# Performance work log

Measured on AMD Instinct MI355X. Metric: run time of the kernel, lower is better.

The kernel has to match this reference:

```python
import jax, jax.numpy as jnp
import numpy as np

N = 20000        # num nodes
E = 600000       # num edges (avg degree 30)
H_DIM = 128      # num_hidden
NUM_IN = 256     # edge feature dim = 2*num_hidden
HEADS = 4
D = H_DIM // HEADS  # per-head dim = 32


def _lin_init(key, out_dim, in_dim):
    return (jax.random.normal(key, (out_dim, in_dim), dtype=jnp.float32)
            * (1.0 / np.sqrt(in_dim)))


def setup_inputs() -> dict:
    key = jax.random.key(0)
    ks = jax.random.split(key, 12)
    h_V = jax.random.normal(ks[0], (N, H_DIM), dtype=jnp.float32)
    h_E = jax.random.normal(ks[1], (E, NUM_IN), dtype=jnp.float32)
    center_id = jax.random.randint(ks[2], (E,), 0, N)
    batch_id = jnp.zeros((N,), dtype=jnp.int32)  # unused by the math
    # W_V: num_in->h, h->h, h->h (GELU between first two pairs)
    Wv1 = _lin_init(ks[3], H_DIM, NUM_IN); bv1 = jnp.zeros((H_DIM,), jnp.float32)
    Wv2 = _lin_init(ks[4], H_DIM, H_DIM);  bv2 = jnp.zeros((H_DIM,), jnp.float32)
    Wv3 = _lin_init(ks[5], H_DIM, H_DIM);  bv3 = jnp.zeros((H_DIM,), jnp.float32)
    # Bias: 3h->h, h->h, h->heads
    Wb1 = _lin_init(ks[6], H_DIM, 3 * H_DIM); bb1 = jnp.zeros((H_DIM,), jnp.float32)
    Wb2 = _lin_init(ks[7], H_DIM, H_DIM);     bb2 = jnp.zeros((H_DIM,), jnp.float32)
    Wb3 = _lin_init(ks[8], HEADS, H_DIM);     bb3 = jnp.zeros((HEADS,), jnp.float32)
    # W_O: h->h, no bias
    Wo = _lin_init(ks[9], H_DIM, H_DIM)
    return {"h_V": h_V, "h_E": h_E,
            "Wv1": Wv1, "bv1": bv1, "Wv2": Wv2, "bv2": bv2, "Wv3": Wv3, "bv3": bv3,
            "Wb1": Wb1, "bb1": bb1, "Wb2": Wb2, "bb2": bb2, "Wb3": Wb3, "bb3": bb3,
            "Wo": Wo, "center_id": center_id, "batch_id": batch_id}


def _gelu(x):
    return jax.nn.gelu(x, approximate=False)  # torch nn.GELU default (erf)


def reference(h_V, h_E, Wv1, bv1, Wv2, bv2, Wv3, bv3,
              Wb1, bb1, Wb2, bb2, Wb3, bb3, Wo, center_id, batch_id):
    n = h_V.shape[0]
    # Bias MLP on gathered node feats + edge feats -> per-edge per-head logit
    x = jnp.concatenate([h_V[center_id], h_E], axis=-1)          # (E, 3h)
    w = _gelu(x @ Wb1.T + bb1)
    w = _gelu(w @ Wb2.T + bb2)
    w = (w @ Wb3.T + bb3) * (1.0 / np.sqrt(D))                   # (E, heads)
    # Value MLP on edge feats
    V = _gelu(h_E @ Wv1.T + bv1)
    V = _gelu(V @ Wv2.T + bv2)
    V = (V @ Wv3.T + bv3).reshape(-1, HEADS, D)                  # (E, heads, d)
    # scatter_softmax over edges sharing a center node
    m = jax.ops.segment_max(w, center_id, num_segments=n)        # (N, heads)
    ew = jnp.exp(w - m[center_id])                               # (E, heads)
    denom = jax.ops.segment_sum(ew, center_id, num_segments=n)   # (N, heads)
    attend = ew / denom[center_id]                               # (E, heads)
    # scatter_sum aggregate of attention-weighted values
    agg = jax.ops.segment_sum(attend[:, :, None] * V, center_id,
                              num_segments=n).reshape(n, H_DIM)  # (N, h)
    return agg @ Wo.T                                            # W_O, no bias
```

## Files before the change

### kernel.cpp

```cpp
#include <hip/hip_runtime.h>
#include <hip/hip_bf16.h>
#include <math.h>

#define TE 32
#define XS 392
#define HS 264
#define NTILES 18750

typedef __attribute__((ext_vector_type(8))) short bf16x8;
typedef __attribute__((ext_vector_type(4))) float f32x4;

__device__ __forceinline__ unsigned short f2b(float f) {
    unsigned int x = __float_as_uint(f);
    unsigned int r = x + 0x7fffu + ((x >> 16) & 1u);
    return (unsigned short)(r >> 16);
}
__device__ __forceinline__ float b2f(unsigned short u) {
    return __uint_as_float(((unsigned int)u) << 16);
}
__device__ __forceinline__ float gelu_exact(float v) {
    return 0.5f * v * (1.0f + erff(v * 0.70710678118654752f));
}

__global__ void __launch_bounds__(256)
k_pre(const float* __restrict__ Wb1, const float* __restrict__ Wb2,
      const float* __restrict__ Wv1, const float* __restrict__ Wv2,
      const float* __restrict__ Wv3, const float* __restrict__ Wo,
      unsigned short* __restrict__ wbf, float* __restrict__ woT) {
    int t = blockIdx.x * 256 + threadIdx.x;
    if (t < 49152)       wbf[t] = f2b(Wb1[t]);
    else if (t < 65536)  wbf[t] = f2b(Wb2[t - 49152]);
    else if (t < 98304)  wbf[t] = f2b(Wv1[t - 65536]);
    else if (t < 114688) wbf[t] = f2b(Wv2[t - 98304]);
    else if (t < 131072) wbf[t] = f2b(Wv3[t - 114688]);
    else if (t < 147456) {
        int i = t - 131072; int j = i >> 7, k = i & 127;
        woT[k * 128 + j] = Wo[j * 128 + k];
    }
}

__global__ void __launch_bounds__(256)
k_hist(const int* __restrict__ center, int* __restrict__ counts) {
    int t = blockIdx.x * 256 + threadIdx.x;
    if (t < 600000) atomicAdd(&counts[center[t]], 1);
}

__global__ void __launch_bounds__(256)
k_scan(const int* __restrict__ counts, int* __restrict__ offsets,
       int* __restrict__ cursor, int n) {
    __shared__ int buf[256];
    __shared__ int carry;
    int t = threadIdx.x;
    if (t == 0) carry = 0;
    __syncthreads();
    for (int base = 0; base < n; base += 256) {
        int v = (base + t < n) ? counts[base + t] : 0;
        buf[t] = v; __syncthreads();
        for (int off = 1; off < 256; off <<= 1) {
            int x = (t >= off) ? buf[t - off] : 0;
            __syncthreads();
            buf[t] += x;
            __syncthreads();
        }
        int excl = carry + buf[t] - v;
        if (base + t < n) { offsets[base + t] = excl; cursor[base + t] = excl; }
        int tot = buf[255];
        __syncthreads();
        if (t == 0) carry += tot;
        __syncthreads();
    }
}

__global__ void __launch_bounds__(256)
k_place(const int* __restrict__ center, int* __restrict__ cursor, int* __restrict__ eidx) {
    int t = blockIdx.x * 256 + threadIdx.x;
    if (t < 600000) {
        int p = atomicAdd(&cursor[center[t]], 1);
        eidx[p] = t;
    }
}

__device__ __forceinline__ void stage_tile(int t, int eg0,
        const float* __restrict__ hE, const float* __restrict__ hV,
        const int* __restrict__ center, unsigned short* __restrict__ xs) {
    #pragma unroll
    for (int i = 0; i < 4; ++i) {
        int vid = t + i * 512;
        int e = vid >> 6, kq = vid & 63;
        float4 g = *(const float4*)(hE + (size_t)(eg0 + e) * 256 + kq * 4);
        ushort4 p; p.x = f2b(g.x); p.y = f2b(g.y); p.z = f2b(g.z); p.w = f2b(g.w);
        *(ushort4*)&xs[e * XS + 128 + kq * 4] = p;
    }
    #pragma unroll
    for (int i = 0; i < 2; ++i) {
        int vid = t + i * 512;
        int e = vid >> 5, kq = vid & 31;
        int c = center[eg0 + e];
        float4 g = *(const float4*)(hV + (size_t)c * 128 + kq * 4);
        ushort4 p; p.x = f2b(g.x); p.y = f2b(g.y); p.z = f2b(g.z); p.w = f2b(g.w);
        *(ushort4*)&xs[e * XS + kq * 4] = p;
    }
}

__global__ void __launch_bounds__(512, 2)
k_edge(const float* __restrict__ hV, const float* __restrict__ hE,
       const int* __restrict__ center,
       const float* __restrict__ bv1, const float* __restrict__ bv2, const float* __restrict__ bv3,
       const float* __restrict__ bb1, const float* __restrict__ bb2,
       const float* __restrict__ Wb3, const float* __restrict__ bb3,
       const unsigned short* __restrict__ wbf,
       unsigned short* __restrict__ Vbf, float* __restrict__ ew, float* __restrict__ denom)
{
    __shared__ unsigned short smem[29440];
    __shared__ float wb3s[512];
    const int t = threadIdx.x;
    const int wave = t >> 6, lane = t & 63;
    const int c16 = lane & 15, q = lane >> 4;
    wb3s[t] = Wb3[t];

    unsigned short* xs = smem;
    unsigned short* h1 = smem + 12544;
    unsigned short* h2 = smem + 20992;

    const unsigned short* Wb1bf = wbf;
    const unsigned short* Wb2bf = wbf + 49152;
    const unsigned short* Wv1bf = wbf + 65536;
    const unsigned short* Wv2bf = wbf + 98304;
    const unsigned short* Wv3bf = wbf + 114688;

    if (wave < 4) {
        const int fb = wave * 32;
        bf16x8 wb1[2][12], wb2[2][4];
        float bias1[2], bias2[2];
        #pragma unroll
        for (int nt = 0; nt < 2; ++nt) {
            const int fr = fb + nt * 16 + c16;
            #pragma unroll
            for (int ks = 0; ks < 12; ++ks)
                wb1[nt][ks] = *(const bf16x8*)(Wb1bf + (size_t)fr * 384 + ks * 32 + q * 8);
            #pragma unroll
            for (int ks = 0; ks < 4; ++ks)
                wb2[nt][ks] = *(const bf16x8*)(Wb2bf + (size_t)fr * 128 + ks * 32 + q * 8);
            bias1[nt] = bb1[fr]; bias2[nt] = bb2[fr];
        }
        for (int tile = blockIdx.x; tile < NTILES; tile += gridDim.x) {
            const int eg0 = tile * TE;
            stage_tile(t, eg0, hE, hV, center, xs);
            __syncthreads();
            #pragma unroll
            for (int m = 0; m < 2; ++m) {
                bf16x8 af[12];
                #pragma unroll
                for (int ks = 0; ks < 12; ++ks)
                    af[ks] = *(const bf16x8*)&xs[(m * 16 + c16) * XS + ks * 32 + q * 8];
                f32x4 a0 = {0.f,0.f,0.f,0.f}, a1 = {0.f,0.f,0.f,0.f};
                #pragma unroll
                for (int ks = 0; ks < 12; ++ks) {
                    a0 = __builtin_amdgcn_mfma_f32_16x16x32_bf16(af[ks], wb1[0][ks], a0, 0, 0, 0);
                    a1 = __builtin_amdgcn_mfma_f32_16x16x32_bf16(af[ks], wb1[1][ks], a1, 0, 0, 0);
                }
                #pragma unroll
                for (int r = 0; r < 4; ++r) {
                    int row = (m * 16 + q * 4 + r) * HS;
                    h1[row + fb + c16]      = f2b(gelu_exact(a0[r] + bias1[0]));
                    h1[row + fb + 16 + c16] = f2b(gelu_exact(a1[r] + bias1[1]));
                }
            }
            __syncthreads();
            #pragma unroll
            for (int m = 0; m < 2; ++m) {
                bf16x8 ah[4];
                #pragma unroll
                for (int ks = 0; ks < 4; ++ks)
                    ah[ks] = *(const bf16x8*)&h1[(m * 16 + c16) * HS + ks * 32 + q * 8];
                f32x4 a0 = {0.f,0.f,0.f,0.f}, a1 = {0.f,0.f,0.f,0.f};
                #pragma unroll
                for (int ks = 0; ks < 4; ++ks) {
                    a0 = __builtin_amdgcn_mfma_f32_16x16x32_bf16(ah[ks], wb2[0][ks], a0, 0, 0, 0);
                    a1 = __builtin_amdgcn_mfma_f32_16x16x32_bf16(ah[ks], wb2[1][ks], a1, 0, 0, 0);
                }
                #pragma unroll
                for (int r = 0; r < 4; ++r) {
                    int row = (m * 16 + q * 4 + r) * HS;
                    h2[row + fb + c16]      = f2b(gelu_exact(a0[r] + bias2[0]));
                    h2[row + fb + 16 + c16] = f2b(gelu_exact(a1[r] + bias2[1]));
                }
            }
            __syncthreads();
            if (t < 128) {
                const int e = t & 31, head = t >> 5;
                float acc = 0.f;
                #pragma unroll
                for (int kc = 0; kc < 16; ++kc) {
                    bf16x8 h = *(const bf16x8*)&h2[e * HS + kc * 8];
                    #pragma unroll
                    for (int j = 0; j < 8; ++j)
                        acc += b2f((unsigned short)h[j]) * wb3s[head * 128 + kc * 8 + j];
                }
                float w = (acc + bb3[head]) * 0.17677669529663689f;
                float xv = expf(w);
                ew[(size_t)(eg0 + e) * 4 + head] = xv;
                atomicAdd(&denom[(size_t)center[eg0 + e] * 4 + head], xv);
            }
        }
    } else {
        const int fv = (wave - 4) * 32;
        bf16x8 wv1[2][8], wv2[2][4], wv3[2][4];
        float bias1[2], bias2[2], bias3[2];
        #pragma unroll
        for (int nt = 0; nt < 2; ++nt) {
            const int fr = fv + nt * 16 + c16;
            #pragma unroll
            for (int ks = 0; ks < 8; ++ks)
                wv1[nt][ks] = *(const bf16x8*)(Wv1bf + (size_t)fr * 256 + ks * 32 + q * 8);
            #pragma unroll
            for (int ks = 0; ks < 4; ++ks) {
                wv2[nt][ks] = *(const bf16x8*)(Wv2bf + (size_t)fr * 128 + ks * 32 + q * 8);
                wv3[nt][ks] = *(const bf16x8*)(Wv3bf + (size_t)fr * 128 + ks * 32 + q * 8);
            }
            bias1[nt] = bv1[fr]; bias2[nt] = bv2[fr]; bias3[nt] = bv3[fr];
        }
        for (int tile = blockIdx.x; tile < NTILES; tile += gridDim.x) {
            const int eg0 = tile * TE;
            stage_tile(t, eg0, hE, hV, center, xs);
            __syncthreads();
            #pragma unroll
            for (int m = 0; m < 2; ++m) {
                bf16x8 af[8];
                #pragma unroll
                for (int ks = 0; ks < 8; ++ks)
                    af[ks] = *(const bf16x8*)&xs[(m * 16 + c16) * XS + 128 + ks * 32 + q * 8];
                f32x4 a0 = {0.f,0.f,0.f,0.f}, a1 = {0.f,0.f,0.f,0.f};
                #pragma unroll
                for (int ks = 0; ks < 8; ++ks) {
                    a0 = __builtin_amdgcn_mfma_f32_16x16x32_bf16(af[ks], wv1[0][ks], a0, 0, 0, 0);
                    a1 = __builtin_amdgcn_mfma_f32_16x16x32_bf16(af[ks], wv1[1][ks], a1, 0, 0, 0);
                }
                #pragma unroll
                for (int r = 0; r < 4; ++r) {
                    int row = (m * 16 + q * 4 + r) * HS;
                    h1[row + 128 + fv + c16]      = f2b(gelu_exact(a0[r] + bias1[0]));
                    h1[row + 128 + fv + 16 + c16] = f2b(gelu_exact(a1[r] + bias1[1]));
                }
            }
            __syncthreads();
            #pragma unroll
            for (int m = 0; m < 2; ++m) {
                bf16x8 ah[4];
                #pragma unroll
                for (int ks = 0; ks < 4; ++ks)
                    ah[ks] = *(const bf16x8*)&h1[(m * 16 + c16) * HS + 128 + ks * 32 + q * 8];
                f32x4 a0 = {0.f,0.f,0.f,0.f}, a1 = {0.f,0.f,0.f,0.f};
                #pragma unroll
                for (int ks = 0; ks < 4; ++ks) {
                    a0 = __builtin_amdgcn_mfma_f32_16x16x32_bf16(ah[ks], wv2[0][ks], a0, 0, 0, 0);
                    a1 = __builtin_amdgcn_mfma_f32_16x16x32_bf16(ah[ks], wv2[1][ks], a1, 0, 0, 0);
                }
                #pragma unroll
                for (int r = 0; r < 4; ++r) {
                    int row = (m * 16 + q * 4 + r) * HS;
                    h2[row + 128 + fv + c16]      = f2b(gelu_exact(a0[r] + bias2[0]));
                    h2[row + 128 + fv + 16 + c16] = f2b(gelu_exact(a1[r] + bias2[1]));
                }
            }
            __syncthreads();
            #pragma unroll
            for (int m = 0; m < 2; ++m) {
                bf16x8 av[4];
                #pragma unroll
                for (int ks = 0; ks < 4; ++ks)
                    av[ks] = *(const bf16x8*)&h2[(m * 16 + c16) * HS + 128 + ks * 32 + q * 8];
                f32x4 a0 = {0.f,0.f,0.f,0.f}, a1 = {0.f,0.f,0.f,0.f};
                #pragma unroll
                for (int ks = 0; ks < 4; ++ks) {
                    a0 = __builtin_amdgcn_mfma_f32_16x16x32_bf16(av[ks], wv3[0][ks], a0, 0, 0, 0);
                    a1 = __builtin_amdgcn_mfma_f32_16x16x32_bf16(av[ks], wv3[1][ks], a1, 0, 0, 0);
                }
                #pragma unroll
                for (int r = 0; r < 4; ++r) {
                    size_t row = (size_t)(eg0 + m * 16 + q * 4 + r) * 128;
                    Vbf[row + fv + c16]      = f2b(a0[r] + bias3[0]);
                    Vbf[row + fv + 16 + c16] = f2b(a1[r] + bias3[1]);
                }
            }
        }
    }
}

__global__ void __launch_bounds__(256)
k_gather_out(const unsigned short* __restrict__ Vbf, const float* __restrict__ ew,
             const float* __restrict__ denom, const int* __restrict__ offsets,
             const int* __restrict__ counts, const int* __restrict__ eidx,
             const float* __restrict__ woT, float* __restrict__ out)
{
    __shared__ float aggs[4][128];
    const int t = threadIdx.x;
    const int node = blockIdx.x * 4 + (t >> 6);
    const int lane = t & 63;
    const int j = lane * 2, head = j >> 5;
    {
        int off = offsets[node], deg = counts[node];
        float den = denom[(size_t)node * 4 + head];
        float dinv = (den != 0.f) ? (1.f / den) : 0.f;
        float a0 = 0.f, a1 = 0.f;
        for (int i = 0; i < deg; ++i) {
            int e = eidx[off + i];
            float at = ew[(size_t)e * 4 + head] * dinv;
            ushort2 v = *(const ushort2*)(Vbf + (size_t)e * 128 + j);
            a0 += at * b2f(v.x);
            a1 += at * b2f(v.y);
        }
        aggs[t >> 6][j]     = a0;
        aggs[t >> 6][j + 1] = a1;
    }
    __syncthreads();
    {
        const int c = t & 127, nh = t >> 7;
        float o0 = 0.f, o1 = 0.f;
        for (int k = 0; k < 128; ++k) {
            float w = woT[k * 128 + c];
            o0 += w * aggs[nh][k];
            o1 += w * aggs[nh + 2][k];
        }
        out[(size_t)(blockIdx.x * 4 + nh) * 128 + c]     = o0;
        out[(size_t)(blockIdx.x * 4 + nh + 2) * 128 + c] = o1;
    }
}

extern "C" void kernel_launch(void* const* d_in, const int* in_sizes, int n_in,
                              void* d_out, int out_size, void* d_ws, size_t ws_size,
                              hipStream_t stream) {
    const float* hV  = (const float*)d_in[0];
    const float* hE  = (const float*)d_in[1];
    const float* Wv1 = (const float*)d_in[2];
    const float* bv1 = (const float*)d_in[3];
    const float* Wv2 = (const float*)d_in[4];
    const float* bv2 = (const float*)d_in[5];
    const float* Wv3 = (const float*)d_in[6];
    const float* bv3 = (const float*)d_in[7];
    const float* Wb1 = (const float*)d_in[8];
    const float* bb1 = (const float*)d_in[9];
    const float* Wb2 = (const float*)d_in[10];
    const float* bb2 = (const float*)d_in[11];
    const float* Wb3 = (const float*)d_in[12];
    const float* bb3 = (const float*)d_in[13];
    const float* Wo  = (const float*)d_in[14];
    const int* center = (const int*)d_in[15];
    float* out = (float*)d_out;

    char* ws = (char*)d_ws;
    unsigned short* wbf = (unsigned short*)(ws + 0);
    float* woT     = (float*)(ws + 262144);
    float* denom   = (float*)(ws + 327680);
    int*   counts  = (int*)  (ws + 647680);
    int*   offsets = (int*)  (ws + 727680);
    int*   cursor  = (int*)  (ws + 807680);
    int*   eidx    = (int*)  (ws + 887680);
    float* ew      = (float*)(ws + 3287680);
    unsigned short* Vbf = (unsigned short*)(ws + 12887680);

    hipMemsetAsync(ws + 327680, 0, 400000, stream);
    k_pre  <<<576, 256, 0, stream>>>(Wb1, Wb2, Wv1, Wv2, Wv3, Wo, wbf, woT);
    k_hist <<<2344, 256, 0, stream>>>(center, counts);
    k_scan <<<1, 256, 0, stream>>>(counts, offsets, cursor, 20000);
    k_place<<<2344, 256, 0, stream>>>(center, cursor, eidx);
    k_edge <<<512, 512, 0, stream>>>(hV, hE, center, bv1, bv2, bv3,
                                     bb1, bb2, Wb3, bb3, wbf, Vbf, ew, denom);
    k_gather_out<<<5000, 256, 0, stream>>>(Vbf, ew, denom, offsets, counts, eidx, woT, out);
}
```

Before: 1.473 ms.

## Precompute per-node bias projection, process edges in sorted order, prefetch tiles, fast GELU

The node half of the first bias layer is precomputed once per node (k_pnode) and gathered per edge, which shrinks the edge GEMM K from 384 to 256 and the staging buffer. Edges are processed in center-sorted order so the aggregation kernel reads V and ew contiguously without the eidx indirection. Next-tile global loads are prefetched into registers, and the bias output layer now uses MFMA. Exact erf GELU is replaced by an Abramowitz-Stegun polynomial, the scan is parallelised, and the occupancy hint and grid size go up. The GELU approximation and bf16 node projection add numerical error, and the gathered edge loads are less coalesced.

```diff
diff --git a/kernel.cpp b/kernel.cpp
--- a/kernel.cpp
+++ b/kernel.cpp
@@ -3,7 +3,7 @@
 #include <math.h>
 
 #define TE 32
-#define XS 392
+#define XS 264
 #define HS 264
 #define NTILES 18750
 
@@ -18,25 +18,58 @@
 __device__ __forceinline__ float b2f(unsigned short u) {
     return __uint_as_float(((unsigned int)u) << 16);
 }
-__device__ __forceinline__ float gelu_exact(float v) {
-    return 0.5f * v * (1.0f + erff(v * 0.70710678118654752f));
+__device__ __forceinline__ float gelu_fast(float v) {
+    float x = fabsf(v) * 0.70710678118654752f;
+    float t = __builtin_amdgcn_rcpf(1.0f + 0.3275911f * x);
+    float p = ((((1.061405429f * t - 1.453152027f) * t + 1.421413741f) * t
+                - 0.284496736f) * t + 0.254829592f) * t;
+    float e = __expf(-x * x);
+    float erfp = 1.0f - p * e;
+    return 0.5f * v * (1.0f + copysignf(erfp, v));
 }
 
 __global__ void __launch_bounds__(256)
 k_pre(const float* __restrict__ Wb1, const float* __restrict__ Wb2,
       const float* __restrict__ Wv1, const float* __restrict__ Wv2,
-      const float* __restrict__ Wv3, const float* __restrict__ Wo,
+      const float* __restrict__ Wv3, const float* __restrict__ Wb3,
+      const float* __restrict__ Wo,
       unsigned short* __restrict__ wbf, float* __restrict__ woT) {
     int t = blockIdx.x * 256 + threadIdx.x;
-    if (t < 49152)       wbf[t] = f2b(Wb1[t]);
-    else if (t < 65536)  wbf[t] = f2b(Wb2[t - 49152]);
-    else if (t < 98304)  wbf[t] = f2b(Wv1[t - 65536]);
-    else if (t < 114688) wbf[t] = f2b(Wv2[t - 98304]);
-    else if (t < 131072) wbf[t] = f2b(Wv3[t - 114688]);
-    else if (t < 147456) {
-        int i = t - 131072; int j = i >> 7, k = i & 127;
+    if (t < 32768) { int f = t >> 8, k = t & 255; wbf[t] = f2b(Wb1[f * 384 + 128 + k]); }
+    else if (t < 49152)  wbf[t] = f2b(Wb2[t - 32768]);
+    else if (t < 81920)  wbf[t] = f2b(Wv1[t - 49152]);
+    else if (t < 98304)  wbf[t] = f2b(Wv2[t - 81920]);
+    else if (t < 114688) wbf[t] = f2b(Wv3[t - 98304]);
+    else if (t < 116736) {
+        int i = t - 114688; int r = i >> 7, k = i & 127;
+        wbf[t] = (r < 4) ? f2b(Wb3[r * 128 + k]) : (unsigned short)0;
+    } else if (t < 133120) {
+        int i = t - 116736; int j = i >> 7, k = i & 127;
         woT[k * 128 + j] = Wo[j * 128 + k];
     }
+}
+
+__global__ void __launch_bounds__(256)
+k_pnode(const float* __restrict__ hV, const float* __restrict__ Wb1,
+        const float* __restrict__ bb1, unsigned short* __restrict__ Pbf) {
+    const int t = threadIdx.x;
+    const int lane = t & 63;
+    const int node = blockIdx.x * 4 + (t >> 6);
+    const int f0 = lane * 2;
+    const float* hv = hV + (size_t)node * 128;
+    const float* w0 = Wb1 + (size_t)f0 * 384;
+    const float* w1 = w0 + 384;
+    float a0 = 0.f, a1 = 0.f;
+    #pragma unroll 4
+    for (int kk = 0; kk < 32; ++kk) {
+        float4 h  = *(const float4*)(hv + kk * 4);
+        float4 x0 = *(const float4*)(w0 + kk * 4);
+        float4 x1 = *(const float4*)(w1 + kk * 4);
+        a0 += h.x * x0.x + h.y * x0.y + h.z * x0.z + h.w * x0.w;
+        a1 += h.x * x1.x + h.y * x1.y + h.z * x1.z + h.w * x1.w;
+    }
+    ushort2 p; p.x = f2b(a0 + bb1[f0]); p.y = f2b(a1 + bb1[f0 + 1]);
+    *(ushort2*)&Pbf[(size_t)node * 128 + f0] = p;
 }
 
 __global__ void __launch_bounds__(256)
@@ -45,29 +78,34 @@
     if (t < 600000) atomicAdd(&counts[center[t]], 1);
 }
 
-__global__ void __launch_bounds__(256)
-k_scan(const int* __restrict__ counts, int* __restrict__ offsets,
-       int* __restrict__ cursor, int n) {
-    __shared__ int buf[256];
-    __shared__ int carry;
-    int t = threadIdx.x;
-    if (t == 0) carry = 0;
+__global__ void __launch_bounds__(1024)
+k_scan(const int* __restrict__ counts, int* __restrict__ cursor, int n) {
+    __shared__ int wtot[16];
+    const int t = threadIdx.x, lane = t & 63, w = t >> 6;
+    const int CH = 20;
+    const int base = t * CH;
+    int loc[CH]; int s = 0;
+    #pragma unroll
+    for (int i = 0; i < CH; ++i) {
+        int idx = base + i;
+        int v = (idx < n) ? counts[idx] : 0;
+        loc[i] = s; s += v;
+    }
+    int inc = s;
+    for (int o = 1; o < 64; o <<= 1) { int u = __shfl_up(inc, o); if (lane >= o) inc += u; }
+    if (lane == 63) wtot[w] = inc;
     __syncthreads();
-    for (int base = 0; base < n; base += 256) {
-        int v = (base + t < n) ? counts[base + t] : 0;
-        buf[t] = v; __syncthreads();
-        for (int off = 1; off < 256; off <<= 1) {
-            int x = (t >= off) ? buf[t - off] : 0;
-            __syncthreads();
-            buf[t] += x;
-            __syncthreads();
-        }
-        int excl = carry + buf[t] - v;
-        if (base + t < n) { offsets[base + t] = excl; cursor[base + t] = excl; }
-        int tot = buf[255];
-        __syncthreads();
-        if (t == 0) carry += tot;
-        __syncthreads();
+    if (w == 0 && lane < 16) {
+        int v = wtot[lane]; int p = v;
+        for (int o = 1; o < 16; o <<= 1) { int u = __shfl_up(p, o); if (lane >= o) p += u; }
+        wtot[lane] = p - v;
+    }
+    __syncthreads();
+    const int excl = wtot[w] + inc - s;
+    #pragma unroll
+    for (int i = 0; i < CH; ++i) {
+        int idx = base + i;
+        if (idx < n) cursor[idx] = excl + loc[i];
     }
 }
 
@@ -80,90 +118,105 @@
     }
 }
 
-__device__ __forceinline__ void stage_tile(int t, int eg0,
-        const float* __restrict__ hE, const float* __restrict__ hV,
-        const int* __restrict__ center, unsigned short* __restrict__ xs) {
-    #pragma unroll
-    for (int i = 0; i < 4; ++i) {
-        int vid = t + i * 512;
-        int e = vid >> 6, kq = vid & 63;
-        float4 g = *(const float4*)(hE + (size_t)(eg0 + e) * 256 + kq * 4);
-        ushort4 p; p.x = f2b(g.x); p.y = f2b(g.y); p.z = f2b(g.z); p.w = f2b(g.w);
-        *(ushort4*)&xs[e * XS + 128 + kq * 4] = p;
-    }
-    #pragma unroll
-    for (int i = 0; i < 2; ++i) {
-        int vid = t + i * 512;
-        int e = vid >> 5, kq = vid & 31;
-        int c = center[eg0 + e];
-        float4 g = *(const float4*)(hV + (size_t)c * 128 + kq * 4);
-        ushort4 p; p.x = f2b(g.x); p.y = f2b(g.y); p.z = f2b(g.z); p.w = f2b(g.w);
-        *(ushort4*)&xs[e * XS + kq * 4] = p;
-    }
-}
-
-__global__ void __launch_bounds__(512, 2)
-k_edge(const float* __restrict__ hV, const float* __restrict__ hE,
-       const int* __restrict__ center,
-       const float* __restrict__ bv1, const float* __restrict__ bv2, const float* __restrict__ bv3,
-       const float* __restrict__ bb1, const float* __restrict__ bb2,
-       const float* __restrict__ Wb3, const float* __restrict__ bb3,
-       const unsigned short* __restrict__ wbf,
+#define PREFETCH(eg) { \
+    int e0_ = eidx[(eg) + wave];      int e1_ = eidx[(eg) + wave + 8]; \
+    int e2_ = eidx[(eg) + wave + 16]; int e3_ = eidx[(eg) + wave + 24]; \
+    if (t < 32) pc = center[eidx[(eg) + t]]; \
+    pre[0] = *(const float4*)(hE + (size_t)e0_ * 256 + kq4); \
+    pre[1] = *(const float4*)(hE + (size_t)e1_ * 256 + kq4); \
+    pre[2] = *(const float4*)(hE + (size_t)e2_ * 256 + kq4); \
+    pre[3] = *(const float4*)(hE + (size_t)e3_ * 256 + kq4); }
+
+#define STAGE() { \
+    _Pragma("unroll") \
+    for (int i_ = 0; i_ < 4; ++i_) { \
+        ushort4 p_; p_.x = f2b(pre[i_].x); p_.y = f2b(pre[i_].y); \
+        p_.z = f2b(pre[i_].z); p_.w = f2b(pre[i_].w); \
+        *(ushort4*)&xs[(wave + i_ * 8) * XS + kq4] = p_; } \
+    if (t < 32) cs[t] = pc; }
+
+__global__ void __launch_bounds__(512, 6)
+k_edge(const float* __restrict__ hE, const int* __restrict__ center,
+       const int* __restrict__ eidx, const unsigned short* __restrict__ Pbf,
+       const float* __restrict__ bv1, const float* __restrict__ bv2,
+       const float* __restrict__ bv3, const float* __restrict__ bb2,
+       const float* __restrict__ bb3, const unsigned short* __restrict__ wbf,
        unsigned short* __restrict__ Vbf, float* __restrict__ ew, float* __restrict__ denom)
 {
-    __shared__ unsigned short smem[29440];
-    __shared__ float wb3s[512];
+    __shared__ unsigned short smem[25344];
+    __shared__ int cs[32];
     const int t = threadIdx.x;
     const int wave = t >> 6, lane = t & 63;
     const int c16 = lane & 15, q = lane >> 4;
-    wb3s[t] = Wb3[t];
+    const int kq4 = (t & 63) * 4;
 
     unsigned short* xs = smem;
-    unsigned short* h1 = smem + 12544;
-    unsigned short* h2 = smem + 20992;
+    unsigned short* h1 = smem + 8448;
+    unsigned short* h2 = smem + 16896;
 
     const unsigned short* Wb1bf = wbf;
-    const unsigned short* Wb2bf = wbf + 49152;
-    const unsigned short* Wv1bf = wbf + 65536;
-    const unsigned short* Wv2bf = wbf + 98304;
-    const unsigned short* Wv3bf = wbf + 114688;
+    const unsigned short* Wb2bf = wbf + 32768;
+    const unsigned short* Wv1bf = wbf + 49152;
+    const unsigned short* Wv2bf = wbf + 81920;
+    const unsigned short* Wv3bf = wbf + 98304;
+    const unsigned short* Wb3bf = wbf + 114688;
+
+    float4 pre[4]; int pc = 0;
+    PREFETCH(blockIdx.x * TE);
 
     if (wave < 4) {
         const int fb = wave * 32;
-        bf16x8 wb1[2][12], wb2[2][4];
-        float bias1[2], bias2[2];
+        bf16x8 wb1r[2][8], wb2r[2][4], wb3f[4];
+        float bias2[2]; float bb3c = 0.f;
         #pragma unroll
         for (int nt = 0; nt < 2; ++nt) {
             const int fr = fb + nt * 16 + c16;
             #pragma unroll
-            for (int ks = 0; ks < 12; ++ks)
-                wb1[nt][ks] = *(const bf16x8*)(Wb1bf + (size_t)fr * 384 + ks * 32 + q * 8);
+            for (int ks = 0; ks < 8; ++ks)
+                wb1r[nt][ks] = *(const bf16x8*)(Wb1bf + (size_t)fr * 256 + ks * 32 + q * 8);
             #pragma unroll
             for (int ks = 0; ks < 4; ++ks)
-                wb2[nt][ks] = *(const bf16x8*)(Wb2bf + (size_t)fr * 128 + ks * 32 + q * 8);
-            bias1[nt] = bb1[fr]; bias2[nt] = bb2[fr];
+                wb2r[nt][ks] = *(const bf16x8*)(Wb2bf + (size_t)fr * 128 + ks * 32 + q * 8);
+            bias2[nt] = bb2[fr];
+        }
+        if (wave == 0) {
+            #pragma unroll
+            for (int ks = 0; ks < 4; ++ks)
+                wb3f[ks] = *(const bf16x8*)(Wb3bf + (size_t)c16 * 128 + ks * 32 + q * 8);
+            bb3c = bb3[c16 & 3];
         }
         for (int tile = blockIdx.x; tile < NTILES; tile += gridDim.x) {
             const int eg0 = tile * TE;
-            stage_tile(t, eg0, hE, hV, center, xs);
-            __syncthreads();
+            STAGE();
+            int nxt = tile + gridDim.x;
+            if (nxt < NTILES) PREFETCH(nxt * TE);
+            __syncthreads();
+            float pva[2][2][4];
+            #pragma unroll
+            for (int m = 0; m < 2; ++m)
+                #pragma unroll
+                for (int r = 0; r < 4; ++r) {
+                    int c = cs[m * 16 + q * 4 + r];
+                    pva[m][0][r] = b2f(Pbf[(size_t)c * 128 + fb + c16]);
+                    pva[m][1][r] = b2f(Pbf[(size_t)c * 128 + fb + 16 + c16]);
+                }
             #pragma unroll
             for (int m = 0; m < 2; ++m) {
-                bf16x8 af[12];
-                #pragma unroll
-                for (int ks = 0; ks < 12; ++ks)
+                bf16x8 af[8];
+                #pragma unroll
+                for (int ks = 0; ks < 8; ++ks)
                     af[ks] = *(const bf16x8*)&xs[(m * 16 + c16) * XS + ks * 32 + q * 8];
                 f32x4 a0 = {0.f,0.f,0.f,0.f}, a1 = {0.f,0.f,0.f,0.f};
                 #pragma unroll
-                for (int ks = 0; ks < 12; ++ks) {
-                    a0 = __builtin_amdgcn_mfma_f32_16x16x32_bf16(af[ks], wb1[0][ks], a0, 0, 0, 0);
-                    a1 = __builtin_amdgcn_mfma_f32_16x16x32_bf16(af[ks], wb1[1][ks], a1, 0, 0, 0);
+                for (int ks = 0; ks < 8; ++ks) {
+                    a0 = __builtin_amdgcn_mfma_f32_16x16x32_bf16(af[ks], wb1r[0][ks], a0, 0, 0, 0);
+                    a1 = __builtin_amdgcn_mfma_f32_16x16x32_bf16(af[ks], wb1r[1][ks], a1, 0, 0, 0);
                 }
                 #pragma unroll
                 for (int r = 0; r < 4; ++r) {
                     int row = (m * 16 + q * 4 + r) * HS;
-                    h1[row + fb + c16]      = f2b(gelu_exact(a0[r] + bias1[0]));
-                    h1[row + fb + 16 + c16] = f2b(gelu_exact(a1[r] + bias1[1]));
+                    h1[row + fb + c16]      = f2b(gelu_fast(a0[r] + pva[m][0][r]));
+                    h1[row + fb + 16 + c16] = f2b(gelu_fast(a1[r] + pva[m][1][r]));
                 }
             }
             __syncthreads();
@@ -176,71 +229,81 @@
                 f32x4 a0 = {0.f,0.f,0.f,0.f}, a1 = {0.f,0.f,0.f,0.f};
                 #pragma unroll
                 for (int ks = 0; ks < 4; ++ks) {
-                    a0 = __builtin_amdgcn_mfma_f32_16x16x32_bf16(ah[ks], wb2[0][ks], a0, 0, 0, 0);
-                    a1 = __builtin_amdgcn_mfma_f32_16x16x32_bf16(ah[ks], wb2[1][ks], a1, 0, 0, 0);
+                    a0 = __builtin_amdgcn_mfma_f32_16x16x32_bf16(ah[ks], wb2r[0][ks], a0, 0, 0, 0);
+                    a1 = __builtin_amdgcn_mfma_f32_16x16x32_bf16(ah[ks], wb2r[1][ks], a1, 0, 0, 0);
                 }
                 #pragma unroll
                 for (int r = 0; r < 4; ++r) {
                     int row = (m * 16 + q * 4 + r) * HS;
-                    h2[row + fb + c16]      = f2b(gelu_exact(a0[r] + bias2[0]));
-                    h2[row + fb + 16 + c16] = f2b(gelu_exact(a1[r] + bias2[1]));
-                }
-            }
-            __syncthreads();
-            if (t < 128) {
-                const int e = t & 31, head = t >> 5;
-                float acc = 0.f;
-                #pragma unroll
-                for (int kc = 0; kc < 16; ++kc) {
-                    bf16x8 h = *(const bf16x8*)&h2[e * HS + kc * 8];
+                    h2[row + fb + c16]      = f2b(gelu_fast(a0[r] + bias2[0]));
+                    h2[row + fb + 16 + c16] = f2b(gelu_fast(a1[r] + bias2[1]));
+                }
+            }
+            __syncthreads();
+            if (wave == 0) {
+                #pragma unroll
+                for (int m = 0; m < 2; ++m) {
+                    bf16x8 ah[4];
                     #pragma unroll
-                    for (int j = 0; j < 8; ++j)
-                        acc += b2f((unsigned short)h[j]) * wb3s[head * 128 + kc * 8 + j];
-                }
-                float w = (acc + bb3[head]) * 0.17677669529663689f;
-                float xv = expf(w);
-                ew[(size_t)(eg0 + e) * 4 + head] = xv;
-                atomicAdd(&denom[(size_t)center[eg0 + e] * 4 + head], xv);
+                    for (int ks = 0; ks < 4; ++ks)
+                        ah[ks] = *(const bf16x8*)&h2[(m * 16 + c16) * HS + ks * 32 + q * 8];
+                    f32x4 a = {0.f,0.f,0.f,0.f};
+                    #pragma unroll
+                    for (int ks = 0; ks < 4; ++ks)
+                        a = __builtin_amdgcn_mfma_f32_16x16x32_bf16(ah[ks], wb3f[ks], a, 0, 0, 0);
+                    if (c16 < 4) {
+                        #pragma unroll
+                        for (int r = 0; r < 4; ++r) {
+                            int row = m * 16 + q * 4 + r;
+                            float wv = (a[r] + bb3c) * 0.17677669529663689f;
+                            float evx = __expf(wv);
+                            ew[(size_t)(eg0 + row) * 4 + c16] = evx;
+                            atomicAdd(&denom[(size_t)cs[row] * 4 + c16], evx);
+                        }
+                    }
+                }
             }
         }
     } else {
         const int fv = (wave - 4) * 32;
-        bf16x8 wv1[2][8], wv2[2][4], wv3[2][4];
-        float bias1[2], bias2[2], bias3[2];
+        bf16x8 wv1r[2][8], wv2r[2][4], wv3r[2][4];
+        float b1[2], b2[2], b3[2];
         #pragma unroll
         for (int nt = 0; nt < 2; ++nt) {
             const int fr = fv + nt * 16 + c16;
             #pragma unroll
             for (int ks = 0; ks < 8; ++ks)
-                wv1[nt][ks] = *(const bf16x8*)(Wv1bf + (size_t)fr * 256 + ks * 32 + q * 8);
+                wv1r[nt][ks] = *(const bf16x8*)(Wv1bf + (size_t)fr * 256 + ks * 32 + q * 8);
             #pragma unroll
             for (int ks = 0; ks < 4; ++ks) {
-                wv2[nt][ks] = *(const bf16x8*)(Wv2bf + (size_t)fr * 128 + ks * 32 + q * 8);
-                wv3[nt][ks] = *(const bf16x8*)(Wv3bf + (size_t)fr * 128 + ks * 32 + q * 8);
-            }
-            bias1[nt] = bv1[fr]; bias2[nt] = bv2[fr]; bias3[nt] = bv3[fr];
+                wv2r[nt][ks] = *(const bf16x8*)(Wv2bf + (size_t)fr * 128 + ks * 32 + q * 8);
+                wv3r[nt][ks] = *(const bf16x8*)(Wv3bf + (size_t)fr * 128 + ks * 32 + q * 8);
+            }
+            b1[nt] = bv1[fr]; b2[nt] = bv2[fr]; b3[nt] = bv3[fr];
         }
         for (int tile = blockIdx.x; tile < NTILES; tile += gridDim.x) {
             const int eg0 = tile * TE;
-            stage_tile(t, eg0, hE, hV, center, xs);
+            STAGE();
+            int nxt = tile + gridDim.x;
+            if (nxt < NTILES) PREFETCH(nxt * TE);
             __syncthreads();
             #pragma unroll
             for (int m = 0; m < 2; ++m) {
                 bf16x8 af[8];
                 #pragma unroll
                 for (int ks = 0; ks < 8; ++ks)
-                    af[ks] = *(const bf16x8*)&xs[(m * 16 + c16) * XS + 128 + ks * 32 + q * 8];
+                    af[ks] = *(const bf16x8*)&xs[(m * 16 + c16) * XS + ks * 32 + q * 8];
                 f32x4 a0 = {0.f,0.f,0.f,0.f}, a1 = {0.f,0.f,0.f,0.f};
                 #pragma unroll
                 for (int ks = 0; ks < 8; ++ks) {
-                    a0 = __builtin_amdgcn_mfma_f32_16x16x32_bf16(af[ks], wv1[0][ks], a0, 0, 0, 0);
-                    a1 = __builtin_amdgcn_mfma_f32_16x16x32_bf16(af[ks], wv1[1][ks], a1, 0, 0, 0);
+                    a0 = __builtin_amdgcn_mfma_f32_16x16x32_bf16(af[ks], wv1r[0][ks], a0, 0, 0, 0);
+                    a1 = __builtin_amdgcn_mfma_f32_16x16x32_bf16(af[ks], wv1r[1][ks], a1, 0, 0, 0);
                 }
                 #pragma unroll
                 for (int r = 0; r < 4; ++r) {
                     int row = (m * 16 + q * 4 + r) * HS;
-                    h1[row + 128 + fv + c16]      = f2b(gelu_exact(a0[r] + bias1[0]));
-                    h1[row + 128 + fv + 16 + c16] = f2b(gelu_exact(a1[r] + bias1[1]));
+                    h1[row + 128 + fv + c16]      = f2b(gelu_fast(a0[r] + b1[0]));
+                    h1[row + 128 + fv + 16 + c16] = f2b(gelu_fast(a1[r] + b1[1]));
                 }
             }
             __syncthreads();
@@ -253,14 +316,14 @@
                 f32x4 a0 = {0.f,0.f,0.f,0.f}, a1 = {0.f,0.f,0.f,0.f};
                 #pragma unroll
                 for (int ks = 0; ks < 4; ++ks) {
-                    a0 = __builtin_amdgcn_mfma_f32_16x16x32_bf16(ah[ks], wv2[0][ks], a0, 0, 0, 0);
-                    a1 = __builtin_amdgcn_mfma_f32_16x16x32_bf16(ah[ks], wv2[1][ks], a1, 0, 0, 0);
+                    a0 = __builtin_amdgcn_mfma_f32_16x16x32_bf16(ah[ks], wv2r[0][ks], a0, 0, 0, 0);
+                    a1 = __builtin_amdgcn_mfma_f32_16x16x32_bf16(ah[ks], wv2r[1][ks], a1, 0, 0, 0);
                 }
                 #pragma unroll
                 for (int r = 0; r < 4; ++r) {
                     int row = (m * 16 + q * 4 + r) * HS;
-                    h2[row + 128 + fv + c16]      = f2b(gelu_exact(a0[r] + bias2[0]));
-                    h2[row + 128 + fv + 16 + c16] = f2b(gelu_exact(a1[r] + bias2[1]));
+                    h2[row + 128 + fv + c16]      = f2b(gelu_fast(a0[r] + b2[0]));
+                    h2[row + 128 + fv + 16 + c16] = f2b(gelu_fast(a1[r] + b2[1]));
                 }
             }
             __syncthreads();
@@ -273,14 +336,14 @@
                 f32x4 a0 = {0.f,0.f,0.f,0.f}, a1 = {0.f,0.f,0.f,0.f};
                 #pragma unroll
                 for (int ks = 0; ks < 4; ++ks) {
-                    a0 = __builtin_amdgcn_mfma_f32_16x16x32_bf16(av[ks], wv3[0][ks], a0, 0, 0, 0);
-                    a1 = __builtin_amdgcn_mfma_f32_16x16x32_bf16(av[ks], wv3[1][ks], a1, 0, 0, 0);
+                    a0 = __builtin_amdgcn_mfma_f32_16x16x32_bf16(av[ks], wv3r[0][ks], a0, 0, 0, 0);
+                    a1 = __builtin_amdgcn_mfma_f32_16x16x32_bf16(av[ks], wv3r[1][ks], a1, 0, 0, 0);
                 }
                 #pragma unroll
                 for (int r = 0; r < 4; ++r) {
                     size_t row = (size_t)(eg0 + m * 16 + q * 4 + r) * 128;
-                    Vbf[row + fv + c16]      = f2b(a0[r] + bias3[0]);
-                    Vbf[row + fv + 16 + c16] = f2b(a1[r] + bias3[1]);
+                    Vbf[row + fv + c16]      = f2b(a0[r] + b3[0]);
+                    Vbf[row + fv + 16 + c16] = f2b(a1[r] + b3[1]);
                 }
             }
         }
@@ -288,30 +351,33 @@
 }
 
 __global__ void __launch_bounds__(256)
-k_gather_out(const unsigned short* __restrict__ Vbf, const float* __restrict__ ew,
-             const float* __restrict__ denom, const int* __restrict__ offsets,
-             const int* __restrict__ counts, const int* __restrict__ eidx,
-             const float* __restrict__ woT, float* __restrict__ out)
+k_agg_out(const unsigned short* __restrict__ Vbf, const float* __restrict__ ew,
+          const float* __restrict__ denom, const int* __restrict__ cursor,
+          const int* __restrict__ counts, const float* __restrict__ woT,
+          float* __restrict__ out)
 {
     __shared__ float aggs[4][128];
     const int t = threadIdx.x;
-    const int node = blockIdx.x * 4 + (t >> 6);
+    const int ln = t >> 6;
+    const int node = blockIdx.x * 4 + ln;
     const int lane = t & 63;
     const int j = lane * 2, head = j >> 5;
     {
-        int off = offsets[node], deg = counts[node];
+        int deg = counts[node];
+        int off = cursor[node] - deg;
         float den = denom[(size_t)node * 4 + head];
         float dinv = (den != 0.f) ? (1.f / den) : 0.f;
+        const unsigned short* vp = Vbf + (size_t)off * 128 + j;
+        const float* ep = ew + (size_t)off * 4 + head;
         float a0 = 0.f, a1 = 0.f;
         for (int i = 0; i < deg; ++i) {
-            int e = eidx[off + i];
-            float at = ew[(size_t)e * 4 + head] * dinv;
-            ushort2 v = *(const ushort2*)(Vbf + (size_t)e * 128 + j);
+            float at = ep[(size_t)i * 4] * dinv;
+            ushort2 v = *(const ushort2*)(vp + (size_t)i * 128);
             a0 += at * b2f(v.x);
             a1 += at * b2f(v.y);
         }
-        aggs[t >> 6][j]     = a0;
-        aggs[t >> 6][j + 1] = a1;
+        aggs[ln][j]     = a0;
+        aggs[ln][j + 1] = a1;
     }
     __syncthreads();
     {
@@ -350,21 +416,22 @@
 
     char* ws = (char*)d_ws;
     unsigned short* wbf = (unsigned short*)(ws + 0);
-    float* woT     = (float*)(ws + 262144);
-    float* denom   = (float*)(ws + 327680);
-    int*   counts  = (int*)  (ws + 647680);
-    int*   offsets = (int*)  (ws + 727680);
-    int*   cursor  = (int*)  (ws + 807680);
-    int*   eidx    = (int*)  (ws + 887680);
-    float* ew      = (float*)(ws + 3287680);
-    unsigned short* Vbf = (unsigned short*)(ws + 12887680);
-
-    hipMemsetAsync(ws + 327680, 0, 400000, stream);
-    k_pre  <<<576, 256, 0, stream>>>(Wb1, Wb2, Wv1, Wv2, Wv3, Wo, wbf, woT);
+    float* woT     = (float*)(ws + 233472);
+    unsigned short* Pbf = (unsigned short*)(ws + 299008);
+    float* denom   = (float*)(ws + 5419008);
+    int*   counts  = (int*)  (ws + 5739008);
+    int*   cursor  = (int*)  (ws + 5819008);
+    int*   eidx    = (int*)  (ws + 5899008);
+    float* ew      = (float*)(ws + 8299008);
+    unsigned short* Vbf = (unsigned short*)(ws + 17899008);
+
+    hipMemsetAsync(ws + 5419008, 0, 400000, stream);
+    k_pre  <<<520, 256, 0, stream>>>(Wb1, Wb2, Wv1, Wv2, Wv3, Wb3, Wo, wbf, woT);
+    k_pnode<<<5000, 256, 0, stream>>>(hV, Wb1, bb1, Pbf);
     k_hist <<<2344, 256, 0, stream>>>(center, counts);
-    k_scan <<<1, 256, 0, stream>>>(counts, offsets, cursor, 20000);
+    k_scan <<<1, 1024, 0, stream>>>(counts, cursor, 20000);
     k_place<<<2344, 256, 0, stream>>>(center, cursor, eidx);
-    k_edge <<<512, 512, 0, stream>>>(hV, hE, center, bv1, bv2, bv3,
-                                     bb1, bb2, Wb3, bb3, wbf, Vbf, ew, denom);
-    k_gather_out<<<5000, 256, 0, stream>>>(Vbf, ew, denom, offsets, counts, eidx, woT, out);
-}
+    k_edge <<<768, 512, 0, stream>>>(hE, center, eidx, Pbf, bv1, bv2, bv3,
+                                     bb2, bb3, wbf, Vbf, ew, denom);
+    k_agg_out<<<5000, 256, 0, stream>>>(Vbf, ew, denom, cursor, counts, woT, out);
+}
```

After: 2.285 ms. 55.1% more time.
